# Optimization experiments

Measured on AMD Instinct MI355X. Metric: run time of the kernel, lower is better.

Reference implementation:

```python
import jax, jax.numpy as jnp
import numpy as np

B, T = 8, 2048
IN, OUT = 1024, 1024
M, C = 32, 32
MIN_P, MAX_P = 1.0, 1024.0
EPS = 1e-5


def setup_inputs() -> dict:
    key = jax.random.key(0)
    ks = jax.random.split(key, 4)
    x = jax.random.normal(ks[0], (B, T, IN), dtype=jnp.float32)
    # pre: Linear(IN, 2*M + 2*OUT); mix: Linear(2*M*C, OUT)
    pre_w = jax.random.normal(ks[1], (IN, 2 * M + 2 * OUT), dtype=jnp.float32) / np.sqrt(IN)
    pre_b = jnp.zeros((2 * M + 2 * OUT,), jnp.float32)
    mix_w = jax.random.normal(ks[2], (2 * M * C, OUT), dtype=jnp.float32) / np.sqrt(2 * M * C)
    mix_b = jnp.zeros((OUT,), jnp.float32)
    # FFA decay/oscillation params (paper init): gamma_{m,c} = exp(-|a_m| + i b_c)
    a = jnp.linspace(1e-6, 0.5, M, dtype=jnp.float32)
    b = 2.0 * jnp.pi / jnp.linspace(MIN_P, MAX_P, C, dtype=jnp.float32)
    return dict(x=x, pre_w=pre_w, pre_b=pre_b, mix_w=mix_w, mix_b=mix_b, a=a, b=b)


def _ffa(u, a, b):
    """Complex-decay linear recurrence: s_t = gamma * s_{t-1} + u_t (s_0 = 0).

    u: [B,T,M] real input (broadcast over context dim C).
    Returns all states: [B,T,M,C] complex64.
    """
    log_gamma = (-jnp.abs(a))[:, None] + 1j * b[None, :]  # [M,C]
    gamma = jnp.exp(log_gamma).astype(jnp.complex64)
    Tn = u.shape[1]
    h = jnp.broadcast_to(u[..., None].astype(jnp.complex64), u.shape + (C,))  # [B,T,M,C]
    h = jnp.moveaxis(h, 1, 0)  # [T,B,M,C]
    p = jnp.broadcast_to(gamma, (Tn, 1, M, C))  # [T,1,M,C] time-invariant decay

    def combine(e1, e2):
        p1, h1 = e1
        p2, h2 = e2
        return (p1 * p2, h1 * p2 + h2)

    _, hs = jax.lax.associative_scan(combine, (p, h), axis=0)
    return jnp.moveaxis(hs, 0, 1)  # [B,T,M,C]


def reference(x, pre_w, pre_b, mix_w, mix_b, a, b):
    Bx, Tx, _ = x.shape
    pre = x @ pre_w + pre_b  # [B,T,2M+2OUT]
    y, thru, gate = jnp.split(pre, [M, M + OUT], axis=-1)
    gate = jax.nn.sigmoid(gate)
    in_gate, out_gate = gate[..., :M], gate[..., M:]
    s = _ffa(y * in_gate, a, b)  # [B,T,M,C] complex64
    # torch.view_as_real -> [...,M,C,2] then flatten -> interleaved (re,im)
    zr = jnp.stack([s.real, s.imag], axis=-1).reshape(Bx, Tx, 2 * M * C)
    z = zr @ mix_w + mix_b  # [B,T,OUT]
    # LayerNorm (no affine)
    z = (z - z.mean(-1, keepdims=True)) / jnp.sqrt(z.var(-1, keepdims=True) + EPS)
    out = z * out_gate + thru * (1.0 - out_gate)
    return out, s
```

## Files before the change

kernel.cpp:

```cpp
#include <hip/hip_runtime.h>
#include <stdint.h>

typedef __attribute__((ext_vector_type(2))) __bf16 bf16x2;
typedef __attribute__((ext_vector_type(4))) __bf16 bf16x4;
typedef __attribute__((ext_vector_type(8))) __bf16 bf16x8;
typedef __attribute__((ext_vector_type(4))) float f32x4;

#define DEV __device__ __forceinline__

DEV void g2lds16(const void* g, void* l) {
  __builtin_amdgcn_global_load_lds(
      (const __attribute__((address_space(1))) void*)g,
      (__attribute__((address_space(3))) void*)l, 16, 0, 0);
}
DEV void bar() {
  asm volatile("" ::: "memory");
  __builtin_amdgcn_s_barrier();
  asm volatile("" ::: "memory");
}
DEV void vm4() { asm volatile("s_waitcnt vmcnt(4)" ::: "memory"); }
DEV void vm0() { asm volatile("s_waitcnt vmcnt(0)" ::: "memory"); }

__global__ __launch_bounds__(256) void cvt_f32_bf16(const float* __restrict__ s,
                                                    __bf16* __restrict__ d, int n) {
  int i = (blockIdx.x * 256 + threadIdx.x) * 4;
  if (i >= n) return;
  float4 v = *reinterpret_cast<const float4*>(s + i);
  bf16x4 o;
  o[0] = (__bf16)v.x; o[1] = (__bf16)v.y; o[2] = (__bf16)v.z; o[3] = (__bf16)v.w;
  *reinterpret_cast<bf16x4*>(d + i) = o;
}

__global__ __launch_bounds__(256) void transpose_to_bf16(const float* __restrict__ src,
                                                         __bf16* __restrict__ dst,
                                                         int K, int N, int Npad) {
  __shared__ float tile[32][33];
  int n0 = blockIdx.x * 32, k0 = blockIdx.y * 32;
  int tx = threadIdx.x & 31, ty = threadIdx.x >> 5;
#pragma unroll
  for (int j = 0; j < 4; ++j) {
    int k = k0 + ty + j * 8;
    int n = n0 + tx;
    float v = 0.f;
    if (n < N) v = src[(long)k * N + n];
    tile[ty + j * 8][tx] = v;
  }
  __syncthreads();
#pragma unroll
  for (int j = 0; j < 4; ++j) {
    int n = n0 + ty + j * 8;
    int k = k0 + tx;
    if (n < Npad) dst[(long)n * K + k] = (__bf16)tile[tx][ty + j * 8];
  }
}

#define STAGE3(BUF, KC)                                              \
  { g2lds16(A + aoffg0 + (KC), &As[BUF][q0 * 8]);                    \
    g2lds16(A + aoffg1 + (KC), &As[BUF][q1 * 8]);                    \
    g2lds16(Wt + boffg0 + (KC), &Bs[BUF][q0 * 8]);                   \
    g2lds16(Wt + boffg1 + (KC), &Bs[BUF][q1 * 8]); }

#define COMPUTE3(CUR)                                                \
  { bf16x8 af[4], bw[4];                                             \
    _Pragma("unroll") for (int i = 0; i < 4; ++i)                    \
        af[i] = *reinterpret_cast<const bf16x8*>(&As[CUR][aoffl[i]]);\
    _Pragma("unroll") for (int n = 0; n < 4; ++n)                    \
        bw[n] = *reinterpret_cast<const bf16x8*>(&Bs[CUR][boffl[n]]);\
    __builtin_amdgcn_s_setprio(1);                                   \
    _Pragma("unroll") for (int i = 0; i < 4; ++i)                    \
      _Pragma("unroll") for (int n = 0; n < 4; ++n)                  \
          acc[i][n] = __builtin_amdgcn_mfma_f32_16x16x32_bf16(       \
              af[i], bw[n], acc[i][n], 0, 0, 0);                     \
    __builtin_amdgcn_s_setprio(0); }

#define ITER3(CUR, STG, KC) \
  STAGE3(STG, KC); COMPUTE3(CUR); vm4(); bar();

template <bool OUT_BF16, int K>
__global__ __launch_bounds__(256, 3) void gemm_p3(const __bf16* __restrict__ A,
                                                  const __bf16* __restrict__ Wt,
                                                  const float* __restrict__ bias,
                                                  void* __restrict__ Cout,
                                                  int Nreal, int ldc, int gx) {
  __shared__ __bf16 As[3][4096];
  __shared__ __bf16 Bs[3][4096];
  const int tid = threadIdx.x;
  const int lane = tid & 63, wid = tid >> 6;

  const int nwg = gridDim.x;
  const int orig = blockIdx.x;
  const int wg = ((orig & 7) * (nwg >> 3)) + (orig >> 3);
  const int tm = (wg / gx) * 128, tn = (wg % gx) * 128;

  f32x4 acc[4][4] = {};

  const int q0 = tid, q1 = tid + 256;
  const int row0 = ((q0 >> 3) << 1) | ((q0 >> 2) & 1);
  const int c0e = (((q0 & 3) - (q0 >> 3)) & 3) * 8;
  const int row1 = row0 + 64;
  const long aoffg0 = (long)(tm + row0) * K + c0e;
  const long aoffg1 = (long)(tm + row1) * K + c0e;
  const long boffg0 = (long)(tn + row0) * K + c0e;
  const long boffg1 = (long)(tn + row1) * K + c0e;

  const int l15 = lane & 15, cl = lane >> 4;
  int aoffl[4], boffl[4];
#pragma unroll
  for (int mf = 0; mf < 4; ++mf) {
    int row = (wid >> 1) * 64 + mf * 16 + l15;
    aoffl[mf] = (row >> 1) * 64 + (((row & 1) << 2) | ((cl + (row >> 1)) & 3)) * 8;
  }
#pragma unroll
  for (int nf = 0; nf < 4; ++nf) {
    int row = (wid & 1) * 64 + nf * 16 + l15;
    boffl[nf] = (row >> 1) * 64 + (((row & 1) << 2) | ((cl + (row >> 1)) & 3)) * 8;
  }

  STAGE3(0, 0);
  STAGE3(1, 32);
  vm4();
  bar();

  if constexpr (K == 1024) {
#pragma unroll 1
    for (int i = 0; i < 10; ++i) {
      const int kc = (3 * i + 2) << 5;
      ITER3(0, 2, kc);
      ITER3(1, 0, kc + 32);
      ITER3(2, 1, kc + 64);
    }
    COMPUTE3(0); vm0(); bar();
    COMPUTE3(1);
  } else {
    ITER3(0, 2, 64);
    ITER3(1, 0, 96);
#pragma unroll 1
    for (int i = 0; i < 20; ++i) {
      const int kc = (3 * i + 4) << 5;
      ITER3(2, 1, kc);
      ITER3(0, 2, kc + 32);
      ITER3(1, 0, kc + 64);
    }
    COMPUTE3(2); vm0(); bar();
    COMPUTE3(0);
  }

#pragma unroll
  for (int mf = 0; mf < 4; ++mf) {
    const int rg = tm + (wid >> 1) * 64 + mf * 16 + (lane >> 4) * 4;
#pragma unroll
    for (int nf = 0; nf < 4; ++nf) {
      int col = tn + (wid & 1) * 64 + nf * 16 + l15;
      if (col < Nreal) {
        float bv = bias[col];
#pragma unroll
        for (int r = 0; r < 4; ++r) {
          long row = rg + r;
          float v = acc[mf][nf][r] + bv;
          if (OUT_BF16) ((__bf16*)Cout)[row * (long)ldc + col] = (__bf16)v;
          else          ((float*)Cout)[row * (long)ldc + col] = v;
        }
      }
    }
  }
}

__global__ __launch_bounds__(256) void u_kernel(const __bf16* __restrict__ pre,
                                                float* __restrict__ u) {
  __shared__ float su[64][33];
  const int b = blockIdx.x >> 5;
  const int t0 = (blockIdx.x & 31) * 64;
  const int tid = threadIdx.x;
  {
    const int r = tid >> 2;
    const int j = (tid & 3) * 8;
    const long rowoff = (long)(b * 2048 + t0 + r) * 2112;
    bf16x8 y8 = *reinterpret_cast<const bf16x8*>(pre + rowoff + j);
    bf16x8 g8 = *reinterpret_cast<const bf16x8*>(pre + rowoff + 1056 + j);
#pragma unroll
    for (int k = 0; k < 8; ++k) {
      float y = (float)y8[k];
      float g = (float)g8[k];
      su[r][j + k] = y / (1.f + expf(-g));
    }
  }
  __syncthreads();
  {
    const int m = tid >> 3;
    const int tt = (tid & 7) * 8;
    float4 o0, o1;
    o0.x = su[tt + 0][m]; o0.y = su[tt + 1][m];
    o0.z = su[tt + 2][m]; o0.w = su[tt + 3][m];
    o1.x = su[tt + 4][m]; o1.y = su[tt + 5][m];
    o1.z = su[tt + 6][m]; o1.w = su[tt + 7][m];
    float* up = u + ((long)(b * 32 + m) * 2048 + t0 + tt);
    *reinterpret_cast<float4*>(up) = o0;
    *reinterpret_cast<float4*>(up + 4) = o1;
  }
}

__global__ __launch_bounds__(64) void scan_kernel(const float* __restrict__ u,
                                                  const float* __restrict__ a,
                                                  const float* __restrict__ bfr,
                                                  __bf16* __restrict__ s_bf,
                                                  float* __restrict__ s_re) {
  int blk = blockIdx.x;
  int b = blk >> 4, mp = blk & 15;
  int lane = threadIdx.x;
  int mh = lane >> 5, c = lane & 31;
  int m = mp * 2 + mh;
  const float* ub = u + (long)(b * 32 + m) * 2048;
  float decay = expf(-fabsf(a[m]));
  float gr = decay * cosf(bfr[c]);
  float gi = decay * sinf(bfr[c]);
  float sr = 0.f, si = 0.f;
  long base = (long)b * 2048 * 1024 + m * 32 + c;
  for (int t = 0; t < 2048; ++t) {
    float uv = ub[t];
    float nr = fmaf(gr, sr, fmaf(-gi, si, uv));
    float ni_ = fmaf(gr, si, gi * sr);
    sr = nr; si = ni_;
    long ci = base + (long)t * 1024;
    bf16x2 zv; zv[0] = (__bf16)sr; zv[1] = (__bf16)si;
    *reinterpret_cast<bf16x2*>(s_bf + 2 * ci) = zv;
    s_re[ci] = sr;
  }
}

__global__ __launch_bounds__(256) void ln_gate_kernel(const __bf16* __restrict__ zb,
                                                      float* __restrict__ out,
                                                      const __bf16* __restrict__ pre) {
  __shared__ float rs[4], rss[4];
  long row = blockIdx.x;
  const __bf16* zp = zb + row * 1024;
  int tid = threadIdx.x;
  bf16x4 zv4 = *reinterpret_cast<const bf16x4*>(zp + tid * 4);
  float v0 = (float)zv4[0], v1 = (float)zv4[1], v2 = (float)zv4[2], v3 = (float)zv4[3];
  float s = v0 + v1 + v2 + v3;
  float ss = v0 * v0 + v1 * v1 + v2 * v2 + v3 * v3;
#pragma unroll
  for (int o = 32; o > 0; o >>= 1) {
    s += __shfl_down(s, o, 64);
    ss += __shfl_down(ss, o, 64);
  }
  if ((tid & 63) == 0) { rs[tid >> 6] = s; rss[tid >> 6] = ss; }
  __syncthreads();
  s = rs[0] + rs[1] + rs[2] + rs[3];
  ss = rss[0] + rss[1] + rss[2] + rss[3];
  float mean = s * (1.f / 1024.f);
  float var = ss * (1.f / 1024.f) - mean * mean;
  float rstd = rsqrtf(var + 1e-5f);
  const __bf16* pr = pre + row * 2112;
  bf16x4 th = *reinterpret_cast<const bf16x4*>(pr + 32 + tid * 4);
  bf16x4 og = *reinterpret_cast<const bf16x4*>(pr + 1088 + tid * 4);
  float4 o; float g;
  g = 1.f / (1.f + expf(-(float)og[0])); o.x = (v0 - mean) * rstd * g + (float)th[0] * (1.f - g);
  g = 1.f / (1.f + expf(-(float)og[1])); o.y = (v1 - mean) * rstd * g + (float)th[1] * (1.f - g);
  g = 1.f / (1.f + expf(-(float)og[2])); o.z = (v2 - mean) * rstd * g + (float)th[2] * (1.f - g);
  g = 1.f / (1.f + expf(-(float)og[3])); o.w = (v3 - mean) * rstd * g + (float)th[3] * (1.f - g);
  *reinterpret_cast<float4*>(out + row * 1024 + tid * 4) = o;
}

extern "C" void kernel_launch(void* const* d_in, const int* in_sizes, int n_in,
                              void* d_out, int out_size, void* d_ws, size_t ws_size,
                              hipStream_t stream) {
  const float* x = (const float*)d_in[0];
  const float* pre_w = (const float*)d_in[1];
  const float* pre_b = (const float*)d_in[2];
  const float* mix_w = (const float*)d_in[3];
  const float* mix_b = (const float*)d_in[4];
  const float* a = (const float*)d_in[5];
  const float* bfr = (const float*)d_in[6];

  char* ws = (char*)d_ws;
  __bf16* buf0  = (__bf16*)(ws + 0);
  __bf16* wtbuf = (__bf16*)(ws + 67108864);
  __bf16* pre   = (__bf16*)(ws + 71827456);
  float*  u     = (float*)(ws + 141033472);
  __bf16* z_bf  = (__bf16*)(ws + 143130624);
  const size_t WS_NEEDED = 176685056ull;
  if (ws_size < WS_NEEDED) return;

  __bf16* x_bf = buf0;
  __bf16* s_bf = buf0;

  float* out0 = (float*)d_out;
  float* s_re = out0 + 16777216;

  cvt_f32_bf16<<<16384, 256, 0, stream>>>(x, x_bf, 16777216);
  transpose_to_bf16<<<dim3(68, 32), 256, 0, stream>>>(pre_w, wtbuf, 1024, 2112, 2176);
  gemm_p3<true, 1024><<<2176, 256, 0, stream>>>(x_bf, wtbuf, pre_b, pre,
                                                2112, 2112, 17);
  u_kernel<<<256, 256, 0, stream>>>(pre, u);
  transpose_to_bf16<<<dim3(32, 64), 256, 0, stream>>>(mix_w, wtbuf, 2048, 1024, 1024);
  scan_kernel<<<128, 64, 0, stream>>>(u, a, bfr, s_bf, s_re);
  gemm_p3<true, 2048><<<1024, 256, 0, stream>>>(s_bf, wtbuf, mix_b, z_bf,
                                                1024, 1024, 8);
  ln_gate_kernel<<<16384, 256, 0, stream>>>(z_bf, out0, pre);
}
```

Baseline: 333.7 us.

## Run mix GEMM in FP8 e4m3 with scaled scan states and weights

The scan now writes its complex states as scaled FP8 e4m3 instead of bf16, and the mix weight is transposed into FP8 with a compensating scale. A new FP8 MFMA GEMM kernel with its own LDS layout replaces the bf16 K=2048 GEMM. This halves the bytes the scan writes and the GEMM reads, and uses the faster FP8 matrix instructions. The cost is lower precision in the mixed output, with some risk of saturation or accuracy loss in the state values.

```diff
diff --git a/kernel.cpp b/kernel.cpp
--- a/kernel.cpp
+++ b/kernel.cpp
@@ -1,4 +1,5 @@
 #include <hip/hip_runtime.h>
+#include <hip/hip_fp8.h>
 #include <stdint.h>
 
 typedef __attribute__((ext_vector_type(2))) __bf16 bf16x2;
@@ -20,6 +21,11 @@
 }
 DEV void vm4() { asm volatile("s_waitcnt vmcnt(4)" ::: "memory"); }
 DEV void vm0() { asm volatile("s_waitcnt vmcnt(0)" ::: "memory"); }
+
+DEV unsigned char to_e4m3(float v) {
+  __hip_fp8_e4m3 f8(v);
+  return *reinterpret_cast<unsigned char*>(&f8);
+}
 
 __global__ __launch_bounds__(256) void cvt_f32_bf16(const float* __restrict__ s,
                                                     __bf16* __restrict__ d, int n) {
@@ -51,6 +57,24 @@
     int n = n0 + ty + j * 8;
     int k = k0 + tx;
     if (n < Npad) dst[(long)n * K + k] = (__bf16)tile[tx][ty + j * 8];
+  }
+}
+
+__global__ __launch_bounds__(256) void transpose_to_fp8(const float* __restrict__ src,
+                                                        unsigned char* __restrict__ dst,
+                                                        int K, int N, float scale) {
+  __shared__ float tile[32][33];
+  int n0 = blockIdx.x * 32, k0 = blockIdx.y * 32;
+  int tx = threadIdx.x & 31, ty = threadIdx.x >> 5;
+#pragma unroll
+  for (int j = 0; j < 4; ++j)
+    tile[ty + j * 8][tx] = src[(long)(k0 + ty + j * 8) * N + n0 + tx];
+  __syncthreads();
+#pragma unroll
+  for (int j = 0; j < 4; ++j) {
+    int n = n0 + ty + j * 8;
+    int k = k0 + tx;
+    dst[(long)n * K + k] = to_e4m3(tile[tx][ty + j * 8] * scale);
   }
 }
 
@@ -76,12 +100,12 @@
 #define ITER3(CUR, STG, KC) \
   STAGE3(STG, KC); COMPUTE3(CUR); vm4(); bar();
 
-template <bool OUT_BF16, int K>
 __global__ __launch_bounds__(256, 3) void gemm_p3(const __bf16* __restrict__ A,
                                                   const __bf16* __restrict__ Wt,
                                                   const float* __restrict__ bias,
-                                                  void* __restrict__ Cout,
+                                                  __bf16* __restrict__ Cout,
                                                   int Nreal, int ldc, int gx) {
+  constexpr int K = 1024;
   __shared__ __bf16 As[3][4096];
   __shared__ __bf16 Bs[3][4096];
   const int tid = threadIdx.x;
@@ -121,29 +145,15 @@
   vm4();
   bar();
 
-  if constexpr (K == 1024) {
 #pragma unroll 1
-    for (int i = 0; i < 10; ++i) {
-      const int kc = (3 * i + 2) << 5;
-      ITER3(0, 2, kc);
-      ITER3(1, 0, kc + 32);
-      ITER3(2, 1, kc + 64);
-    }
-    COMPUTE3(0); vm0(); bar();
-    COMPUTE3(1);
-  } else {
-    ITER3(0, 2, 64);
-    ITER3(1, 0, 96);
-#pragma unroll 1
-    for (int i = 0; i < 20; ++i) {
-      const int kc = (3 * i + 4) << 5;
-      ITER3(2, 1, kc);
-      ITER3(0, 2, kc + 32);
-      ITER3(1, 0, kc + 64);
-    }
-    COMPUTE3(2); vm0(); bar();
-    COMPUTE3(0);
-  }
+  for (int i = 0; i < 10; ++i) {
+    const int kc = (3 * i + 2) << 5;
+    ITER3(0, 2, kc);
+    ITER3(1, 0, kc + 32);
+    ITER3(2, 1, kc + 64);
+  }
+  COMPUTE3(0); vm0(); bar();
+  COMPUTE3(1);
 
 #pragma unroll
   for (int mf = 0; mf < 4; ++mf) {
@@ -154,13 +164,112 @@
       if (col < Nreal) {
         float bv = bias[col];
 #pragma unroll
-        for (int r = 0; r < 4; ++r) {
-          long row = rg + r;
-          float v = acc[mf][nf][r] + bv;
-          if (OUT_BF16) ((__bf16*)Cout)[row * (long)ldc + col] = (__bf16)v;
-          else          ((float*)Cout)[row * (long)ldc + col] = v;
-        }
+        for (int r = 0; r < 4; ++r)
+          Cout[(long)(rg + r) * ldc + col] = (__bf16)(acc[mf][nf][r] + bv);
       }
+    }
+  }
+}
+
+#define STAGEF8(BUF, KC)                                             \
+  { g2lds16(A + aoffg0 + (KC), &As[BUF][q0 * 16]);                   \
+    g2lds16(A + aoffg1 + (KC), &As[BUF][q1 * 16]);                   \
+    g2lds16(Wt + boffg0 + (KC), &Bs[BUF][q0 * 16]);                  \
+    g2lds16(Wt + boffg1 + (KC), &Bs[BUF][q1 * 16]); }
+
+#define COMPUTEF8(CUR)                                                        \
+  { long long af[4][2], bw[4][2];                                             \
+    _Pragma("unroll") for (int i = 0; i < 4; ++i)                             \
+      _Pragma("unroll") for (int k = 0; k < 2; ++k) {                         \
+        af[i][k] = *reinterpret_cast<const long long*>(&As[CUR][aoffl[i][k]]);\
+        bw[i][k] = *reinterpret_cast<const long long*>(&Bs[CUR][boffl[i][k]]);\
+      }                                                                       \
+    __builtin_amdgcn_s_setprio(1);                                            \
+    _Pragma("unroll") for (int k = 0; k < 2; ++k)                             \
+      _Pragma("unroll") for (int i = 0; i < 4; ++i)                           \
+        _Pragma("unroll") for (int n = 0; n < 4; ++n)                         \
+            acc[i][n] = __builtin_amdgcn_mfma_f32_16x16x32_fp8_fp8(           \
+                af[i][k], bw[n][k], acc[i][n], 0, 0, 0);                      \
+    __builtin_amdgcn_s_setprio(0); }
+
+#define ITERF8(CUR, STG, KC) \
+  STAGEF8(STG, KC); COMPUTEF8(CUR); vm4(); bar();
+
+__global__ __launch_bounds__(256, 3) void gemm_f8(const unsigned char* __restrict__ A,
+                                                  const unsigned char* __restrict__ Wt,
+                                                  const float* __restrict__ bias,
+                                                  __bf16* __restrict__ Cout,
+                                                  int ldc, int gx) {
+  constexpr int K = 2048;
+  __shared__ unsigned char As[3][8192];
+  __shared__ unsigned char Bs[3][8192];
+  const int tid = threadIdx.x;
+  const int lane = tid & 63, wid = tid >> 6;
+
+  const int nwg = gridDim.x;
+  const int orig = blockIdx.x;
+  const int wg = ((orig & 7) * (nwg >> 3)) + (orig >> 3);
+  const int tm = (wg / gx) * 128, tn = (wg % gx) * 128;
+
+  f32x4 acc[4][4] = {};
+
+  const int q0 = tid, q1 = tid + 256;
+  const int row0 = ((q0 >> 3) << 1) | ((q0 >> 2) & 1);
+  const int c0e = (((q0 & 3) - (q0 >> 3)) & 3) * 16;
+  const int row1 = row0 + 64;
+  const long aoffg0 = (long)(tm + row0) * K + c0e;
+  const long aoffg1 = (long)(tm + row1) * K + c0e;
+  const long boffg0 = (long)(tn + row0) * K + c0e;
+  const long boffg1 = (long)(tn + row1) * K + c0e;
+
+  const int l15 = lane & 15, cl = lane >> 4;
+  int aoffl[4][2], boffl[4][2];
+#pragma unroll
+  for (int mf = 0; mf < 4; ++mf) {
+    int row = (wid >> 1) * 64 + mf * 16 + l15;
+#pragma unroll
+    for (int ks = 0; ks < 2; ++ks) {
+      int sc = ks * 2 + (cl >> 1);
+      aoffl[mf][ks] = ((row >> 1) * 8 + ((row & 1) << 2) + ((sc + (row >> 1)) & 3)) * 16 +
+                      (cl & 1) * 8;
+    }
+  }
+#pragma unroll
+  for (int nf = 0; nf < 4; ++nf) {
+    int row = (wid & 1) * 64 + nf * 16 + l15;
+#pragma unroll
+    for (int ks = 0; ks < 2; ++ks) {
+      int sc = ks * 2 + (cl >> 1);
+      boffl[nf][ks] = ((row >> 1) * 8 + ((row & 1) << 2) + ((sc + (row >> 1)) & 3)) * 16 +
+                      (cl & 1) * 8;
+    }
+  }
+
+  STAGEF8(0, 0);
+  STAGEF8(1, 64);
+  vm4();
+  bar();
+
+#pragma unroll 1
+  for (int i = 0; i < 10; ++i) {
+    const int kc = (3 * i + 2) << 6;
+    ITERF8(0, 2, kc);
+    ITERF8(1, 0, kc + 64);
+    ITERF8(2, 1, kc + 128);
+  }
+  COMPUTEF8(0); vm0(); bar();
+  COMPUTEF8(1);
+
+#pragma unroll
+  for (int mf = 0; mf < 4; ++mf) {
+    const int rg = tm + (wid >> 1) * 64 + mf * 16 + (lane >> 4) * 4;
+#pragma unroll
+    for (int nf = 0; nf < 4; ++nf) {
+      int col = tn + (wid & 1) * 64 + nf * 16 + l15;
+      float bv = bias[col];
+#pragma unroll
+      for (int r = 0; r < 4; ++r)
+        Cout[(long)(rg + r) * ldc + col] = (__bf16)(acc[mf][nf][r] + bv);
     }
   }
 }
@@ -202,7 +311,7 @@
 __global__ __launch_bounds__(64) void scan_kernel(const float* __restrict__ u,
                                                   const float* __restrict__ a,
                                                   const float* __restrict__ bfr,
-                                                  __bf16* __restrict__ s_bf,
+                                                  unsigned char* __restrict__ s_f8,
                                                   float* __restrict__ s_re) {
   int blk = blockIdx.x;
   int b = blk >> 4, mp = blk & 15;
@@ -221,8 +330,10 @@
     float ni_ = fmaf(gr, si, gi * sr);
     sr = nr; si = ni_;
     long ci = base + (long)t * 1024;
-    bf16x2 zv; zv[0] = (__bf16)sr; zv[1] = (__bf16)si;
-    *reinterpret_cast<bf16x2*>(s_bf + 2 * ci) = zv;
+    uchar2 p;
+    p.x = to_e4m3(sr * 0.5f);
+    p.y = to_e4m3(si * 0.5f);
+    *reinterpret_cast<uchar2*>(s_f8 + 2 * ci) = p;
     s_re[ci] = sr;
   }
 }
@@ -282,19 +393,18 @@
   if (ws_size < WS_NEEDED) return;
 
   __bf16* x_bf = buf0;
-  __bf16* s_bf = buf0;
+  unsigned char* s_f8 = (unsigned char*)buf0;
+  unsigned char* mixWT_f8 = (unsigned char*)wtbuf;
 
   float* out0 = (float*)d_out;
   float* s_re = out0 + 16777216;
 
   cvt_f32_bf16<<<16384, 256, 0, stream>>>(x, x_bf, 16777216);
   transpose_to_bf16<<<dim3(68, 32), 256, 0, stream>>>(pre_w, wtbuf, 1024, 2112, 2176);
-  gemm_p3<true, 1024><<<2176, 256, 0, stream>>>(x_bf, wtbuf, pre_b, pre,
-                                                2112, 2112, 17);
+  gemm_p3<<<2176, 256, 0, stream>>>(x_bf, wtbuf, pre_b, pre, 2112, 2112, 17);
   u_kernel<<<256, 256, 0, stream>>>(pre, u);
-  transpose_to_bf16<<<dim3(32, 64), 256, 0, stream>>>(mix_w, wtbuf, 2048, 1024, 1024);
-  scan_kernel<<<128, 64, 0, stream>>>(u, a, bfr, s_bf, s_re);
-  gemm_p3<true, 2048><<<1024, 256, 0, stream>>>(s_bf, wtbuf, mix_b, z_bf,
-                                                1024, 1024, 8);
+  transpose_to_fp8<<<dim3(32, 64), 256, 0, stream>>>(mix_w, mixWT_f8, 2048, 1024, 2.0f);
+  scan_kernel<<<128, 64, 0, stream>>>(u, a, bfr, s_f8, s_re);
+  gemm_f8<<<1024, 256, 0, stream>>>(s_f8, mixWT_f8, mix_b, z_bf, 1024, 8);
   ln_gate_kernel<<<16384, 256, 0, stream>>>(z_bf, out0, pre);
 }
```

After: 363.5 us. 8.9% more time.
